# Kernel optimization log

Hardware: AMD Instinct MI355X
Metric: run time of the kernel (lower is better)

Reference implementation:

```python
import jax, jax.numpy as jnp
import numpy as np

Q = 3  # q_order: SelfONN concatenates powers x^1..x^Q on channel dim

def selfonn_conv(x, w, b, pad):
    # x: (B, C, H, W); w: (O, C*Q, kh, kw); b: (O,)
    xp = jnp.concatenate([x ** (i + 1) for i in range(Q)], axis=1)
    y = jax.lax.conv_general_dilated(
        xp, w, window_strides=(1, 1), padding=[(pad, pad), (pad, pad)],
        dimension_numbers=("NCHW", "OIHW", "NCHW"))
    return y + b[None, :, None, None]

def setup_inputs() -> dict:
    key = jax.random.key(0)
    ks = jax.random.split(key, 9)
    B, C, H, W = 4, 64, 64, 64
    P = 64  # pab_channels
    s1 = 1.0 / np.sqrt(C * Q)          # 1x1 convs
    s3 = 1.0 / np.sqrt(C * Q * 9)      # 3x3 convs
    return {
        "x": jax.random.normal(ks[0], (B, C, H, W), jnp.float32),
        "top_w": jax.random.normal(ks[1], (P, C * Q, 1, 1), jnp.float32) * s1,
        "top_b": jnp.zeros((P,), jnp.float32),
        "center_w": jax.random.normal(ks[2], (P, C * Q, 1, 1), jnp.float32) * s1,
        "center_b": jnp.zeros((P,), jnp.float32),
        "bottom_w": jax.random.normal(ks[3], (C, C * Q, 3, 3), jnp.float32) * s3,
        "bottom_b": jnp.zeros((C,), jnp.float32),
        "out_w": jax.random.normal(ks[4], (C, C * Q, 3, 3), jnp.float32) * s3,
        "out_b": jnp.zeros((C,), jnp.float32),
    }

def reference(x, top_w, top_b, center_w, center_b, bottom_w, bottom_b, out_w, out_b):
    B, C, H, W = x.shape
    HW = H * W
    x_top = selfonn_conv(x, top_w, top_b, 0).reshape(B, -1, HW)            # (B, P, HW)
    x_center = selfonn_conv(x, center_w, center_b, 0).reshape(B, -1, HW)  # (B, P, HW)
    x_bottom = selfonn_conv(x, bottom_w, bottom_b, 1).reshape(B, C, HW)   # (B, C, HW)
    x_center = jnp.swapaxes(x_center, 1, 2)  # (B, HW, P)
    x_bottom = jnp.swapaxes(x_bottom, 1, 2)  # (B, HW, C)
    sp = jnp.einsum("bnp,bpm->bnm", x_center, x_top)  # (B, HW, HW)
    # GLOBAL softmax over the entire HW*HW map per sample (dim=1 on flattened view)
    sp = jax.nn.softmax(sp.reshape(B, -1), axis=1).reshape(B, HW, HW)
    sp = jnp.einsum("bnm,bmc->bnc", sp, x_bottom)  # (B, HW, C)
    # faithful to torch: raw reshape (B, HW, C) -> (B, C, H, W), no transpose
    sp = sp.reshape(B, C, H, W)
    return selfonn_conv(x + sp, out_w, out_b, 1)
```

## Files before the change

### kernel.cpp

```cpp
#include <hip/hip_runtime.h>
#include <hip/hip_bf16.h>

namespace {
constexpr int IMG    = 262144;
constexpr int PADIMG = 4356;
constexpr float LOG2E = 1.44269504088896340736f;
constexpr int WBFO  = 0;
constexpr int XPADO = 122880;
constexpr int TOPO  = 1795584;
constexpr int CENO  = 2319872;
constexpr int BOTO  = 2844160;
constexpr int PVO   = 3368448;
constexpr int MSO4  = 5465600;
constexpr int MSO8  = 7562752;
constexpr size_t NEED8 = (size_t)(MSO8 + 8192) * 4;
}

using half8v  = __attribute__((ext_vector_type(8))) _Float16;
using half4v  = __attribute__((ext_vector_type(4))) _Float16;
using short8v = __attribute__((ext_vector_type(8))) short;
using short4v = __attribute__((ext_vector_type(4))) short;
using uint4v  = __attribute__((ext_vector_type(4))) unsigned;
typedef __attribute__((ext_vector_type(4))) float f32x4;

__device__ __forceinline__ short f2bf(float f) {
    __hip_bfloat16 h = __float2bfloat16(f);
    return *reinterpret_cast<short*>(&h);
}
__device__ __forceinline__ float bf2f(short s) {
    unsigned u = ((unsigned)(unsigned short)s) << 16;
    return __uint_as_float(u);
}
__device__ __forceinline__ unsigned pkrtz(float a, float b) {
    return __builtin_bit_cast(unsigned, __builtin_amdgcn_cvt_pkrtz(a, b));
}

__global__ __launch_bounds__(256) void k_prep(const float* __restrict__ bw, const float* __restrict__ ow,
                                              const float* __restrict__ tw, const float* __restrict__ cw,
                                              _Float16* __restrict__ wbf,
                                              const float* __restrict__ x, _Float16* __restrict__ xpad) {
    __shared__ float xs[64 * 65];
    int bx = blockIdx.x, t = threadIdx.x;
    if (bx < 960) {
        int idx = bx * 256 + t;
        if (idx < 221184) {
            int tsel = idx / 110592;
            int r    = idx - tsel * 110592;
            int tap  = r / 12288;
            int rr   = r - tap * 12288;
            int ck   = rr / 2048;
            int r2   = rr - ck * 2048;
            int o    = r2 >> 5;
            int ki   = r2 & 31;
            int k    = ck * 32 + ki;
            int p    = k >> 6, ci = k & 63;
            const float* src = tsel ? ow : bw;
            wbf[idx] = (_Float16)src[o * 1728 + (p * 64 + ci) * 9 + tap];
        } else {
            int j = idx - 221184;
            int tsel = j / 12288;
            int rr   = j - tsel * 12288;
            int ck   = rr / 2048;
            int r2   = rr - ck * 2048;
            int o    = r2 >> 5;
            int ki   = r2 & 31;
            int k    = ck * 32 + ki;
            wbf[idx] = (_Float16)(tsel ? cw[o * 192 + k] * LOG2E : tw[o * 192 + k]);
        }
        return;
    }
    int bx2 = bx - 960;
    int b = bx2 >> 6, h = bx2 & 63;
    {
        _Float16* base = xpad + (size_t)b * 6 * PADIMG * 32;
        int px[6];
        px[0] = (h + 1) * 66;
        px[1] = (h + 1) * 66 + 65;
        px[2] = h;
        px[3] = 65 * 66 + h;
        int npx = 4;
        if (h < 2) { px[4] = 64 + h; px[5] = 65 * 66 + 64 + h; npx = 6; }
        int pi = t / 24, ck = t % 24;
        if (pi < npx) {
            int cp = ck >> 2, q = ck & 3;
            half8v z = {0, 0, 0, 0, 0, 0, 0, 0};
            *(half8v*)&base[((size_t)cp * PADIMG + px[pi]) * 32 + q * 8] = z;
        }
    }
    #pragma unroll
    for (int it = 0; it < 16; ++it) {
        int idx = it * 256 + t;
        int ci = idx >> 6, wc = idx & 63;
        xs[ci * 65 + wc] = x[b * IMG + ci * 4096 + h * 64 + wc];
    }
    __syncthreads();
    _Float16* dst = xpad + ((size_t)b * 6 * PADIMG + (h + 1) * 66 + 1) * 32;
    #pragma unroll
    for (int it = 0; it < 6; ++it) {
        int u = it * 256 + t;
        int ck = u >> 8, within = u & 255;
        int px = within >> 2, q = within & 3;
        int k0 = ck * 32 + q * 8;
        int p = k0 >> 6, c0 = k0 & 63;
        half8v o;
        #pragma unroll
        for (int j = 0; j < 8; ++j) {
            float v = xs[(c0 + j) * 65 + px];
            float pw = (p == 0) ? v : ((p == 1) ? v * v : v * v * v);
            o[j] = (_Float16)pw;
        }
        *(half8v*)&dst[((size_t)ck * PADIMG + px) * 32 + q * 8] = o;
    }
}

__device__ __forceinline__ void conv3d32(int bx, int t,
                                         const _Float16* __restrict__ src,
                                         const _Float16* __restrict__ wt,
                                         const float* __restrict__ bias,
                                         _Float16* __restrict__ dh_, float* __restrict__ df) {
    int lane = t & 63, w = t >> 6;
    int l16 = lane & 15, quad = lane >> 4;
    int oh = bx >> 8, mt = bx & 255;
    int b = mt >> 6, h = mt & 63;
    const _Float16* abase = src + ((size_t)b * 6 * PADIMG + (h + 1) * 66 + 1 + w * 16 + l16) * 32 + quad * 8;
    const _Float16* bbase = wt + (size_t)(oh * 32 + l16) * 32 + quad * 8;
    f32x4 acc[2];
    acc[0] = (f32x4){0.f, 0.f, 0.f, 0.f};
    acc[1] = (f32x4){0.f, 0.f, 0.f, 0.f};
    for (int tap = 0; tap < 9; ++tap) {
        int dh = tap / 3 - 1, dw = tap % 3 - 1;
        const _Float16* arow = abase + (dh * 66 + dw) * 32;
        const _Float16* brow = bbase + (size_t)tap * 6 * 2048;
        #pragma unroll
        for (int c6 = 0; c6 < 6; ++c6) {
            half8v afr  = *(const half8v*)&arow[(size_t)c6 * PADIMG * 32];
            half8v bfr0 = *(const half8v*)&brow[(size_t)c6 * 2048];
            half8v bfr1 = *(const half8v*)&brow[(size_t)c6 * 2048 + 512];
            acc[0] = __builtin_amdgcn_mfma_f32_16x16x32_f16(afr, bfr0, acc[0], 0, 0, 0);
            acc[1] = __builtin_amdgcn_mfma_f32_16x16x32_f16(afr, bfr1, acc[1], 0, 0, 0);
        }
    }
    #pragma unroll
    for (int nf = 0; nf < 2; ++nf) {
        int c = oh * 32 + nf * 16 + l16;
        float bv = bias[c];
        size_t oi = (size_t)b * 262144 + (size_t)c * 4096 + h * 64 + w * 16 + quad * 4;
        if (dh_) {
            half4v o;
            #pragma unroll
            for (int r = 0; r < 4; ++r) o[r] = (_Float16)(acc[nf][r] + bv);
            *(half4v*)&dh_[oi] = o;
        } else {
            float4 o = make_float4(acc[nf][0] + bv, acc[nf][1] + bv, acc[nf][2] + bv, acc[nf][3] + bv);
            *(float4*)&df[oi] = o;
        }
    }
}

__global__ __launch_bounds__(256) void k_convs(const _Float16* __restrict__ xpad,
                                               const _Float16* __restrict__ wbf,
                                               const float* __restrict__ tb, const float* __restrict__ cb,
                                               const float* __restrict__ bbias,
                                               _Float16* __restrict__ topd, _Float16* __restrict__ cend,
                                               _Float16* __restrict__ botb) {
    int bx = blockIdx.x, t = threadIdx.x;
    if (bx < 512) {
        conv3d32(bx, t, xpad, wbf , bbias, botb, nullptr);
        return;
    }
    int bx2 = bx - 512;
    int lane = t & 63, w = t >> 6;
    int l16 = lane & 15, quad = lane >> 4;
    int ot = bx2 >> 8, mt = bx2 & 255;
    int b = mt >> 6, h = mt & 63;
    const _Float16* wt   = wbf + (ot ? 233472 : 221184);
    const float*    bias = ot ? cb : tb;
    _Float16*       dst  = (ot ? cend : topd) + (size_t)b * IMG;
    const _Float16* abase = xpad + ((size_t)b * 6 * PADIMG + (h + 1) * 66 + 1 + w * 16 + l16) * 32 + quad * 8;
    const _Float16* bbase = wt + (size_t)l16 * 32 + quad * 8;
    f32x4 acc[4];
    #pragma unroll
    for (int nf = 0; nf < 4; ++nf) acc[nf] = (f32x4){0.f, 0.f, 0.f, 0.f};
    #pragma unroll
    for (int kc = 0; kc < 6; ++kc) {
        half8v afr = *(const half8v*)&abase[(size_t)kc * PADIMG * 32];
        #pragma unroll
        for (int nf = 0; nf < 4; ++nf) {
            half8v bfr = *(const half8v*)&bbase[(size_t)kc * 2048 + nf * 16 * 32];
            acc[nf] = __builtin_amdgcn_mfma_f32_16x16x32_f16(afr, bfr, acc[nf], 0, 0, 0);
        }
    }
    _Float16* dp = dst + (size_t)(h * 64 + w * 16) * 64;
    #pragma unroll
    for (int nf = 0; nf < 4; ++nf) {
        float bv = bias[nf * 16 + l16];
        if (ot) bv *= LOG2E;
        #pragma unroll
        for (int r = 0; r < 4; ++r)
            dp[(quad * 4 + r) * 64 + nf * 16 + l16] = (_Float16)(acc[nf][r] + bv);
    }
}

__global__ __launch_bounds__(256) void k_attn(float* __restrict__ ws, int mtiles, int msoOff, int zsoOff) {
    __shared__ _Float16 ltop[64 * 72];
    __shared__ _Float16 lbot[64 * 72];
    int t    = threadIdx.x;
    int lane = t & 63, w = t >> 6;
    int l16  = lane & 15, quad = lane >> 4;
    bool hi16 = (lane & 16) != 0;
    int bxr = blockIdx.x;
    int bx  = (bxr & 7) * ((int)gridDim.x >> 3) + (bxr >> 3);
    int st = bx & 31, b = (bx >> 5) & 3, s = bx >> 7;
    int n0 = st * 128;
    int mbase = s * mtiles * 64;
    const _Float16* topg = (const _Float16*)(ws + TOPO) + (size_t)b * IMG;
    const _Float16* ceng = (const _Float16*)(ws + CENO) + (size_t)b * IMG;
    const _Float16* botg = (const _Float16*)(ws + BOTO) + (size_t)b * IMG;

    half8v bcen[2][2];
    #pragma unroll
    for (int nj = 0; nj < 2; ++nj)
        #pragma unroll
        for (int kk = 0; kk < 2; ++kk)
            bcen[nj][kk] = *(const half8v*)&ceng[(size_t)(n0 + w * 32 + nj * 16 + l16) * 64 + kk * 32 + quad * 8];

    int r0 = t >> 3, r1 = r0 + 32, off = (t & 7) * 8;

    f32x4 pv[4][2];
    #pragma unroll
    for (int cj = 0; cj < 4; ++cj)
        #pragma unroll
        for (int nj = 0; nj < 2; ++nj) pv[cj][nj] = (f32x4){0.f, 0.f, 0.f, 0.f};
    float runm = -3.0e38f, zacc = 0.f;

    half8v rt0 = *(const half8v*)&topg[(size_t)(mbase + r0) * 64 + off];
    half8v rt1 = *(const half8v*)&topg[(size_t)(mbase + r1) * 64 + off];
    half8v rb0 = *(const half8v*)&botg[(size_t)r0 * 4096 + mbase + off];
    half8v rb1 = *(const half8v*)&botg[(size_t)r1 * 4096 + mbase + off];

    for (int tt = 0; tt < mtiles; ++tt) {
        __syncthreads();
        *(half8v*)&ltop[r0 * 72 + off] = rt0;
        *(half8v*)&ltop[r1 * 72 + off] = rt1;
        *(half8v*)&lbot[r0 * 72 + off] = rb0;
        *(half8v*)&lbot[r1 * 72 + off] = rb1;
        __syncthreads();
        if (tt < mtiles - 1) {
            int m1 = mbase + (tt + 1) * 64;
            rt0 = *(const half8v*)&topg[(size_t)(m1 + r0) * 64 + off];
            rt1 = *(const half8v*)&topg[(size_t)(m1 + r1) * 64 + off];
            rb0 = *(const half8v*)&botg[(size_t)r0 * 4096 + m1 + off];
            rb1 = *(const half8v*)&botg[(size_t)r1 * 4096 + m1 + off];
        }
        f32x4 sa[4][2];
        #pragma unroll
        for (int mi = 0; mi < 4; ++mi)
            #pragma unroll
            for (int nj = 0; nj < 2; ++nj) sa[mi][nj] = (f32x4){0.f, 0.f, 0.f, 0.f};
        __builtin_amdgcn_s_setprio(1);
        #pragma unroll
        for (int kk = 0; kk < 2; ++kk)
            #pragma unroll
            for (int mi = 0; mi < 4; ++mi) {
                half8v at = *(half8v*)&ltop[(mi * 16 + l16) * 72 + kk * 32 + quad * 8];
                sa[mi][0] = __builtin_amdgcn_mfma_f32_16x16x32_f16(at, bcen[0][kk], sa[mi][0], 0, 0, 0);
                sa[mi][1] = __builtin_amdgcn_mfma_f32_16x16x32_f16(at, bcen[1][kk], sa[mi][1], 0, 0, 0);
            }
        __builtin_amdgcn_s_setprio(0);
        float lm = -3.0e38f;
        #pragma unroll
        for (int mi = 0; mi < 4; ++mi)
            #pragma unroll
            for (int nj = 0; nj < 2; ++nj) {
                float a = fmaxf(sa[mi][nj][0], sa[mi][nj][1]);
                float c2 = fmaxf(sa[mi][nj][2], sa[mi][nj][3]);
                lm = fmaxf(lm, fmaxf(a, c2));
            }
        if (!__all(lm - runm <= 8.0f)) {
            float tm = lm;
            for (int o2 = 32; o2; o2 >>= 1) tm = fmaxf(tm, __shfl_xor(tm, o2, 64));
            if (tm > runm) {
                float sc = __builtin_amdgcn_exp2f(runm - tm);
                zacc *= sc;
                #pragma unroll
                for (int cj = 0; cj < 4; ++cj)
                    #pragma unroll
                    for (int nj = 0; nj < 2; ++nj) pv[cj][nj] *= sc;
                runm = tm;
            }
        }
        #pragma unroll
        for (int kb = 0; kb < 2; ++kb) {
            unsigned pk[2][2][2];
            #pragma unroll
            for (int f = 0; f < 2; ++f) {
                int mi = 2 * kb + f;
                #pragma unroll
                for (int nj = 0; nj < 2; ++nj) {
                    float e0 = __builtin_amdgcn_exp2f(sa[mi][nj][0] - runm);
                    float e1 = __builtin_amdgcn_exp2f(sa[mi][nj][1] - runm);
                    float e2 = __builtin_amdgcn_exp2f(sa[mi][nj][2] - runm);
                    float e3 = __builtin_amdgcn_exp2f(sa[mi][nj][3] - runm);
                    zacc += (e0 + e1) + (e2 + e3);
                    pk[f][nj][0] = pkrtz(e0, e1);
                    pk[f][nj][1] = pkrtz(e2, e3);
                }
            }
            half8v pa[2];
            #pragma unroll
            for (int nj = 0; nj < 2; ++nj) {
                unsigned T[4];
                #pragma unroll
                for (int d = 0; d < 2; ++d) {
                    unsigned X = pk[0][nj][d], Y = pk[1][nj][d];
                    asm("v_permlane32_swap_b32 %0, %1" : "+v"(X), "+v"(Y));
                    unsigned A0s = __builtin_amdgcn_ds_swizzle(X, 0x401F);
                    unsigned A1s = __builtin_amdgcn_ds_swizzle(Y, 0x401F);
                    T[d]     = hi16 ? A1s : X;
                    T[d + 2] = hi16 ? Y : A0s;
                }
                uint4v tv = {T[0], T[1], T[2], T[3]};
                pa[nj] = __builtin_bit_cast(half8v, tv);
            }
            __builtin_amdgcn_s_setprio(1);
            #pragma unroll
            for (int cj = 0; cj < 4; ++cj) {
                half8v ab = *(half8v*)&lbot[(cj * 16 + l16) * 72 + kb * 32 + quad * 8];
                pv[cj][0] = __builtin_amdgcn_mfma_f32_16x16x32_f16(ab, pa[0], pv[cj][0], 0, 0, 0);
                pv[cj][1] = __builtin_amdgcn_mfma_f32_16x16x32_f16(ab, pa[1], pv[cj][1], 0, 0, 0);
            }
            __builtin_amdgcn_s_setprio(0);
        }
    }
    for (int o2 = 32; o2; o2 >>= 1) zacc += __shfl_xor(zacc, o2, 64);
    if (lane == 0) {
        ws[msoOff + s * 512 + b * 128 + st * 4 + w] = runm;
        ws[zsoOff + s * 512 + b * 128 + st * 4 + w] = zacc;
    }
    short* pvp = (short*)(ws + PVO) + (size_t)s * 1048576 + (size_t)b * IMG;
    #pragma unroll
    for (int cj = 0; cj < 4; ++cj)
        #pragma unroll
        for (int nj = 0; nj < 2; ++nj) {
            short4v o;
            #pragma unroll
            for (int r = 0; r < 4; ++r) o[r] = f2bf(pv[cj][nj][r]);
            *(short4v*)&pvp[(size_t)(n0 + w * 32 + nj * 16 + l16) * 64 + cj * 16 + quad * 4] = o;
        }
}

__global__ __launch_bounds__(512) void k_finalu(const float* __restrict__ x, float* __restrict__ ws,
                                                _Float16* __restrict__ upad,
                                                int ms, int msoOff, int zsoOff) {
    __shared__ float us[64 * 65];
    __shared__ float rm[8], rz[8];
    int t = threadIdx.x, bx = blockIdx.x;
    int b = bx >> 6, h = bx & 63;
    int g = t & 127;
    float m = -3.0e38f;
    for (int s = 0; s < ms; ++s)
        m = fmaxf(m, ws[msoOff + s * 512 + b * 128 + g]);
    for (int o2 = 32; o2; o2 >>= 1) m = fmaxf(m, __shfl_xor(m, o2, 64));
    if ((t & 63) == 0) rm[t >> 6] = m;
    __syncthreads();
    float M = rm[0];
    #pragma unroll
    for (int j = 1; j < 8; ++j) M = fmaxf(M, rm[j]);
    float z = 0.f;
    if (t < 128) {
        for (int s = 0; s < ms; ++s)
            z += ws[zsoOff + s * 512 + b * 128 + g] *
                 __builtin_amdgcn_exp2f(ws[msoOff + s * 512 + b * 128 + g] - M);
    }
    for (int o2 = 32; o2; o2 >>= 1) z += __shfl_xor(z, o2, 64);
    if ((t & 63) == 0) rz[t >> 6] = z;
    __syncthreads();
    float Z = 0.f;
    #pragma unroll
    for (int j = 0; j < 8; ++j) Z += rz[j];
    float rZ = 1.0f / Z;

    const short* pvb = (const short*)(ws + PVO) + (size_t)b * IMG;
    int hg = h >> 5;
    {
        int idx = t * 8;
        int ci = idx >> 6, wc = idx & 63;
        int rem = ci * 4096 + h * 64 + wc;
        int grp = ci * 2 + hg;
        float acc[8] = {};
        for (int s = 0; s < ms; ++s) {
            float scl = __builtin_amdgcn_exp2f(ws[msoOff + s * 512 + b * 128 + grp] - M);
            short8v pvv = *(const short8v*)&pvb[(size_t)s * 1048576 + rem];
            #pragma unroll
            for (int i = 0; i < 8; ++i) acc[i] += bf2f(pvv[i]) * scl;
        }
        float4 x0 = *(const float4*)&x[(size_t)b * IMG + rem];
        float4 x1 = *(const float4*)&x[(size_t)b * IMG + rem + 4];
        float xv[8] = {x0.x, x0.y, x0.z, x0.w, x1.x, x1.y, x1.z, x1.w};
        #pragma unroll
        for (int i = 0; i < 8; ++i)
            us[ci * 65 + wc + i] = xv[i] + acc[i] * rZ;
    }
    __syncthreads();
    _Float16* dst = upad + ((size_t)b * 6 * PADIMG + (h + 1) * 66 + 1) * 32;
    #pragma unroll
    for (int it = 0; it < 3; ++it) {
        int u = it * 512 + t;
        int ck = u >> 8, within = u & 255;
        int px = within >> 2, q = within & 3;
        int k0 = ck * 32 + q * 8;
        int p = k0 >> 6, c0 = k0 & 63;
        half8v o;
        #pragma unroll
        for (int j = 0; j < 8; ++j) {
            float v = us[(c0 + j) * 65 + px];
            float pw = (p == 0) ? v : ((p == 1) ? v * v : v * v * v);
            o[j] = (_Float16)pw;
        }
        *(half8v*)&dst[((size_t)ck * PADIMG + px) * 32 + q * 8] = o;
    }
}

__global__ __launch_bounds__(256) void k_conv3o(const _Float16* __restrict__ upad,
                                                const _Float16* __restrict__ wout,
                                                const float* __restrict__ ob,
                                                float* __restrict__ out) {
    conv3d32(blockIdx.x, threadIdx.x, upad, wout, ob, nullptr, out);
}

extern "C" void kernel_launch(void* const* d_in, const int* in_sizes, int n_in,
                              void* d_out, int out_size, void* d_ws, size_t ws_size,
                              hipStream_t stream) {
    (void)in_sizes; (void)n_in; (void)out_size;
    const float* x  = (const float*)d_in[0];
    const float* tw = (const float*)d_in[1];
    const float* tb = (const float*)d_in[2];
    const float* cw = (const float*)d_in[3];
    const float* cb = (const float*)d_in[4];
    const float* bw = (const float*)d_in[5];
    const float* bb = (const float*)d_in[6];
    const float* ow = (const float*)d_in[7];
    const float* ob = (const float*)d_in[8];
    float* ws  = (float*)d_ws;
    float* out = (float*)d_out;

    _Float16* wbf  = (_Float16*)(ws + WBFO);
    _Float16* wout = wbf + 110592;
    _Float16* xpad = (_Float16*)(ws + XPADO);
    _Float16* topb = (_Float16*)(ws + TOPO);
    _Float16* cenb = (_Float16*)(ws + CENO);
    _Float16* botb = (_Float16*)(ws + BOTO);

    int ms     = (ws_size >= NEED8) ? 8 : 4;
    int mtiles = 64 / ms;
    int msoOff = (ms == 8) ? MSO8 : MSO4;
    int zsoOff = msoOff + ms * 512;

    hipLaunchKernelGGL(k_prep, dim3(1216), dim3(256), 0, stream, bw, ow, tw, cw, wbf, x, xpad);
    hipLaunchKernelGGL(k_convs, dim3(1024), dim3(256), 0, stream, xpad, wbf, tb, cb, bb, topb, cenb, botb);
    hipLaunchKernelGGL(k_attn, dim3(128 * ms), dim3(256), 0, stream, ws, mtiles, msoOff, zsoOff);
    hipLaunchKernelGGL(k_finalu, dim3(256), dim3(512), 0, stream, x, ws, xpad, ms, msoOff, zsoOff);
    hipLaunchKernelGGL(k_conv3o, dim3(512), dim3(256), 0, stream, xpad, wout, ob, out);
}
```

Measured before the change: 167.7 us.

## Load attention tiles straight from global into MFMA fragments, dropping LDS staging

The attention kernel stops staging top and bottom tiles through shared memory with barriers. Each wave now loads its MFMA operand fragments directly from global memory, relying on L1/L2 for reuse across the four waves. The m-tile loop is templated and fully unrolled, with launch bounds asking for 4 blocks per CU. The softmax denominator now accumulates via fdot2 on the fp16-packed exponentials rather than fp32 adds. This removes LDS traffic and syncs but multiplies global/cache load traffic per block, and sums the normaliser in rounded fp16 values.

```diff
diff --git a/kernel.cpp b/kernel.cpp
--- a/kernel.cpp
+++ b/kernel.cpp
@@ -18,6 +18,7 @@
 
 using half8v  = __attribute__((ext_vector_type(8))) _Float16;
 using half4v  = __attribute__((ext_vector_type(4))) _Float16;
+using fp16x2  = __attribute__((ext_vector_type(2))) __fp16;
 using short8v = __attribute__((ext_vector_type(8))) short;
 using short4v = __attribute__((ext_vector_type(4))) short;
 using uint4v  = __attribute__((ext_vector_type(4))) unsigned;
@@ -201,9 +202,8 @@
     }
 }
 
-__global__ __launch_bounds__(256) void k_attn(float* __restrict__ ws, int mtiles, int msoOff, int zsoOff) {
-    __shared__ _Float16 ltop[64 * 72];
-    __shared__ _Float16 lbot[64 * 72];
+template<int MT>
+__global__ __launch_bounds__(256, 4) void k_attn(float* __restrict__ ws, int msoOff, int zsoOff) {
     int t    = threadIdx.x;
     int lane = t & 63, w = t >> 6;
     int l16  = lane & 15, quad = lane >> 4;
@@ -212,7 +212,7 @@
     int bx  = (bxr & 7) * ((int)gridDim.x >> 3) + (bxr >> 3);
     int st = bx & 31, b = (bx >> 5) & 3, s = bx >> 7;
     int n0 = st * 128;
-    int mbase = s * mtiles * 64;
+    int mbase = s * MT * 64;
     const _Float16* topg = (const _Float16*)(ws + TOPO) + (size_t)b * IMG;
     const _Float16* ceng = (const _Float16*)(ws + CENO) + (size_t)b * IMG;
     const _Float16* botg = (const _Float16*)(ws + BOTO) + (size_t)b * IMG;
@@ -224,7 +224,8 @@
         for (int kk = 0; kk < 2; ++kk)
             bcen[nj][kk] = *(const half8v*)&ceng[(size_t)(n0 + w * 32 + nj * 16 + l16) * 64 + kk * 32 + quad * 8];
 
-    int r0 = t >> 3, r1 = r0 + 32, off = (t & 7) * 8;
+    const _Float16* topA = topg + (size_t)(mbase + l16) * 64 + quad * 8;
+    const _Float16* botA = botg + (size_t)l16 * 4096 + mbase + quad * 8;
 
     f32x4 pv[4][2];
     #pragma unroll
@@ -232,47 +233,39 @@
         #pragma unroll
         for (int nj = 0; nj < 2; ++nj) pv[cj][nj] = (f32x4){0.f, 0.f, 0.f, 0.f};
     float runm = -3.0e38f, zacc = 0.f;
-
-    half8v rt0 = *(const half8v*)&topg[(size_t)(mbase + r0) * 64 + off];
-    half8v rt1 = *(const half8v*)&topg[(size_t)(mbase + r1) * 64 + off];
-    half8v rb0 = *(const half8v*)&botg[(size_t)r0 * 4096 + mbase + off];
-    half8v rb1 = *(const half8v*)&botg[(size_t)r1 * 4096 + mbase + off];
-
-    for (int tt = 0; tt < mtiles; ++tt) {
-        __syncthreads();
-        *(half8v*)&ltop[r0 * 72 + off] = rt0;
-        *(half8v*)&ltop[r1 * 72 + off] = rt1;
-        *(half8v*)&lbot[r0 * 72 + off] = rb0;
-        *(half8v*)&lbot[r1 * 72 + off] = rb1;
-        __syncthreads();
-        if (tt < mtiles - 1) {
-            int m1 = mbase + (tt + 1) * 64;
-            rt0 = *(const half8v*)&topg[(size_t)(m1 + r0) * 64 + off];
-            rt1 = *(const half8v*)&topg[(size_t)(m1 + r1) * 64 + off];
-            rb0 = *(const half8v*)&botg[(size_t)r0 * 4096 + m1 + off];
-            rb1 = *(const half8v*)&botg[(size_t)r1 * 4096 + m1 + off];
-        }
+#if __has_builtin(__builtin_amdgcn_fdot2)
+    const fp16x2 one2 = {(__fp16)1.0f, (__fp16)1.0f};
+#endif
+
+    #pragma unroll
+    for (int tt = 0; tt < MT; ++tt) {
+        const _Float16* tA = topA + tt * 4096;
+        const _Float16* bA = botA + tt * 64;
         f32x4 sa[4][2];
         #pragma unroll
         for (int mi = 0; mi < 4; ++mi)
             #pragma unroll
             for (int nj = 0; nj < 2; ++nj) sa[mi][nj] = (f32x4){0.f, 0.f, 0.f, 0.f};
-        __builtin_amdgcn_s_setprio(1);
-        #pragma unroll
-        for (int kk = 0; kk < 2; ++kk)
+        #pragma unroll
+        for (int kk = 0; kk < 2; ++kk) {
+            half8v at[4];
+            #pragma unroll
+            for (int mi = 0; mi < 4; ++mi)
+                at[mi] = *(const half8v*)&tA[mi * 1024 + kk * 32];
+            __builtin_amdgcn_s_setprio(1);
             #pragma unroll
             for (int mi = 0; mi < 4; ++mi) {
-                half8v at = *(half8v*)&ltop[(mi * 16 + l16) * 72 + kk * 32 + quad * 8];
-                sa[mi][0] = __builtin_amdgcn_mfma_f32_16x16x32_f16(at, bcen[0][kk], sa[mi][0], 0, 0, 0);
-                sa[mi][1] = __builtin_amdgcn_mfma_f32_16x16x32_f16(at, bcen[1][kk], sa[mi][1], 0, 0, 0);
-            }
-        __builtin_amdgcn_s_setprio(0);
+                sa[mi][0] = __builtin_amdgcn_mfma_f32_16x16x32_f16(at[mi], bcen[0][kk], sa[mi][0], 0, 0, 0);
+                sa[mi][1] = __builtin_amdgcn_mfma_f32_16x16x32_f16(at[mi], bcen[1][kk], sa[mi][1], 0, 0, 0);
+            }
+            __builtin_amdgcn_s_setprio(0);
+        }
         float lm = -3.0e38f;
         #pragma unroll
         for (int mi = 0; mi < 4; ++mi)
             #pragma unroll
             for (int nj = 0; nj < 2; ++nj) {
-                float a = fmaxf(sa[mi][nj][0], sa[mi][nj][1]);
+                float a  = fmaxf(sa[mi][nj][0], sa[mi][nj][1]);
                 float c2 = fmaxf(sa[mi][nj][2], sa[mi][nj][3]);
                 lm = fmaxf(lm, fmaxf(a, c2));
             }
@@ -301,9 +294,14 @@
                     float e1 = __builtin_amdgcn_exp2f(sa[mi][nj][1] - runm);
                     float e2 = __builtin_amdgcn_exp2f(sa[mi][nj][2] - runm);
                     float e3 = __builtin_amdgcn_exp2f(sa[mi][nj][3] - runm);
-                    zacc += (e0 + e1) + (e2 + e3);
                     pk[f][nj][0] = pkrtz(e0, e1);
                     pk[f][nj][1] = pkrtz(e2, e3);
+#if __has_builtin(__builtin_amdgcn_fdot2)
+                    zacc = __builtin_amdgcn_fdot2(__builtin_bit_cast(fp16x2, pk[f][nj][0]), one2, zacc, false);
+                    zacc = __builtin_amdgcn_fdot2(__builtin_bit_cast(fp16x2, pk[f][nj][1]), one2, zacc, false);
+#else
+                    zacc += (e0 + e1) + (e2 + e3);
+#endif
                 }
             }
             half8v pa[2];
@@ -322,12 +320,15 @@
                 uint4v tv = {T[0], T[1], T[2], T[3]};
                 pa[nj] = __builtin_bit_cast(half8v, tv);
             }
+            half8v ab[4];
+            #pragma unroll
+            for (int cj = 0; cj < 4; ++cj)
+                ab[cj] = *(const half8v*)&bA[cj * 65536 + kb * 32];
             __builtin_amdgcn_s_setprio(1);
             #pragma unroll
             for (int cj = 0; cj < 4; ++cj) {
-                half8v ab = *(half8v*)&lbot[(cj * 16 + l16) * 72 + kb * 32 + quad * 8];
-                pv[cj][0] = __builtin_amdgcn_mfma_f32_16x16x32_f16(ab, pa[0], pv[cj][0], 0, 0, 0);
-                pv[cj][1] = __builtin_amdgcn_mfma_f32_16x16x32_f16(ab, pa[1], pv[cj][1], 0, 0, 0);
+                pv[cj][0] = __builtin_amdgcn_mfma_f32_16x16x32_f16(ab[cj], pa[0], pv[cj][0], 0, 0, 0);
+                pv[cj][1] = __builtin_amdgcn_mfma_f32_16x16x32_f16(ab[cj], pa[1], pv[cj][1], 0, 0, 0);
             }
             __builtin_amdgcn_s_setprio(0);
         }
@@ -452,13 +453,15 @@
     _Float16* botb = (_Float16*)(ws + BOTO);
 
     int ms     = (ws_size >= NEED8) ? 8 : 4;
-    int mtiles = 64 / ms;
     int msoOff = (ms == 8) ? MSO8 : MSO4;
     int zsoOff = msoOff + ms * 512;
 
     hipLaunchKernelGGL(k_prep, dim3(1216), dim3(256), 0, stream, bw, ow, tw, cw, wbf, x, xpad);
     hipLaunchKernelGGL(k_convs, dim3(1024), dim3(256), 0, stream, xpad, wbf, tb, cb, bb, topb, cenb, botb);
-    hipLaunchKernelGGL(k_attn, dim3(128 * ms), dim3(256), 0, stream, ws, mtiles, msoOff, zsoOff);
+    if (ms == 8)
+        hipLaunchKernelGGL(k_attn<8>,  dim3(1024), dim3(256), 0, stream, ws, msoOff, zsoOff);
+    else
+        hipLaunchKernelGGL(k_attn<16>, dim3(512),  dim3(256), 0, stream, ws, msoOff, zsoOff);
     hipLaunchKernelGGL(k_finalu, dim3(256), dim3(512), 0, stream, x, ws, xpad, ms, msoOff, zsoOff);
     hipLaunchKernelGGL(k_conv3o, dim3(512), dim3(256), 0, stream, xpad, wout, ob, out);
 }
```

Result: slower. 194.6 us (+16.0%).
